# Kernel tuning notes

Measured on AMD Instinct MI355X. Metric: run time of the kernel, lower is better.

The kernel has to match this reference:

```python
import jax, jax.numpy as jnp
import numpy as np

B, S = 32, 10  # hard-coded in original call()/reshape


def setup_inputs() -> dict:
    key = jax.random.key(0)
    k1, k2, k3 = jax.random.split(key, 3)
    D, K = 4096, 8192
    p = jax.random.normal(k1, (B, S, D), dtype=jnp.float32)
    q = jax.random.normal(k2, (B, S, D), dtype=jnp.float32)
    W = jax.random.uniform(k3, (K, D), dtype=jnp.float32)  # 'uniform' initializer
    return {"p": p, "q": q, "W": W}


def reference(p, q, W):
    # Multi-perspective matching: for each perspective k, weight p rows and the
    # last q state by W[k], then cosine distance = -mean(l2norm(a)*l2norm(b)).
    # Vectorized over (batch, perspective, seq) via einsums on W^2 -- never
    # materializes the (B,K,S,D) weighted tensors.
    D = p.shape[-1]
    W2 = W * W                                   # (K, D)
    q_last = q[:, -1, :]                          # (B, D)
    # dot(w*q_last, w*p_s) = sum_d p*q_last*W^2
    dot = jnp.einsum('bsd,kd->bks', p * q_last[:, None, :], W2)   # (B, K, S)
    norm_p = jnp.sqrt(jnp.einsum('bsd,kd->bks', p * p, W2))       # (B, K, S)
    norm_q = jnp.sqrt(jnp.einsum('bd,kd->bk', q_last * q_last, W2))  # (B, K)
    dist = -dot / (norm_p * norm_q[:, :, None] * D)  # -mean of normalized product
    # original concatenates over k then s per batch, then reshapes to (32,10,K)
    return dist.reshape(B, S, -1)
```

## Files before the change

kernel.cpp:

```cpp
#include <hip/hip_runtime.h>
#include <stdint.h>

#define B_ 32
#define S_ 10
#define D_ 4096
#define K_ 8192
#define RPB 21
#define M_REAL (B_ * RPB)

#define BM 128
#define BN 128
#define BK 32
#define M_PAD_MF 768
#define KSPLIT 2
#define KHALF (D_ / KSPLIT)
#define NSTEP (KHALF / BK)

typedef _Float16 f16x8 __attribute__((ext_vector_type(8)));
typedef float f32x4 __attribute__((ext_vector_type(4)));
typedef unsigned short us4 __attribute__((ext_vector_type(4)));

__device__ __forceinline__ void async16(const void* g, void* l) {
  __builtin_amdgcn_global_load_lds(
      (const __attribute__((address_space(1))) unsigned int*)g,
      (__attribute__((address_space(3))) unsigned int*)l, 16, 0, 0);
}

__global__ __launch_bounds__(256)
void build_a_f16(const float* __restrict__ p, const float* __restrict__ q,
                 unsigned short* __restrict__ Af) {
  size_t idx = (size_t)blockIdx.x * 256 + threadIdx.x;
  int d4 = (int)(idx & 1023);
  int m = (int)(idx >> 10);
  float4 v = make_float4(0.f, 0.f, 0.f, 0.f);
  if (m < M_REAL) {
    int b = m / RPB;
    int r = m - b * RPB;
    const float4* q4 = (const float4*)(q + (size_t)(b * S_ + (S_ - 1)) * D_);
    if (r < S_) {
      const float4* p4 = (const float4*)(p + (size_t)(b * S_ + r) * D_);
      float4 pv = p4[d4]; float4 qv = q4[d4];
      v = make_float4(pv.x * qv.x, pv.y * qv.y, pv.z * qv.z, pv.w * qv.w);
    } else if (r < 2 * S_) {
      const float4* p4 = (const float4*)(p + (size_t)(b * S_ + (r - S_)) * D_);
      float4 pv = p4[d4];
      v = make_float4(pv.x * pv.x, pv.y * pv.y, pv.z * pv.z, pv.w * pv.w);
    } else {
      float4 qv = q4[d4];
      v = make_float4(qv.x * qv.x, qv.y * qv.y, qv.z * qv.z, qv.w * qv.w);
    }
  }
  us4 h;
  ((unsigned short*)&h)[0] = (unsigned short)__builtin_bit_cast(unsigned short, (_Float16)v.x);
  ((unsigned short*)&h)[1] = (unsigned short)__builtin_bit_cast(unsigned short, (_Float16)v.y);
  ((unsigned short*)&h)[2] = (unsigned short)__builtin_bit_cast(unsigned short, (_Float16)v.z);
  ((unsigned short*)&h)[3] = (unsigned short)__builtin_bit_cast(unsigned short, (_Float16)v.w);
  ((us4*)Af)[idx] = h;
}

__global__ __launch_bounds__(256, 4)
void gemm_mfma(const unsigned short* __restrict__ Af, const float* __restrict__ W,
               float* __restrict__ G) {
  __shared__ unsigned short lds[24576];
  const int tid = threadIdx.x;
  const int lane = tid & 63;
  const int wid = tid >> 6;
  const int m0 = blockIdx.y * BM;
  const int n0 = blockIdx.x * BN;
  const int ks = blockIdx.z;
  const int d_base = ks * KHALF;

  char* const ldsb = (char*)lds;
  char* const ldsWf = ldsb + 16384;

  const unsigned short* gpA[2];
  uint32_t ldsoffA[2];
#pragma unroll
  for (int half = 0; half < 2; ++half) {
    int row = half * 64 + wid * 16 + (lane >> 2);
    int g = (lane & 3) ^ ((row ^ (row >> 2)) & 3);
    gpA[half] = Af + (size_t)(m0 + row) * D_ + d_base + g * 8;
    ldsoffA[half] = (uint32_t)(half * 4096 + wid * 1024);
  }

  const float* gpW[4];
  uint32_t ldsoffW[4];
#pragma unroll
  for (int e = 0; e < 4; ++e) {
    int row = wid * 32 + e * 8 + (lane >> 3);
    int g = (lane & 7) ^ (row & 7);
    gpW[e] = W + (size_t)(n0 + row) * D_ + d_base + g * 4;
    ldsoffW[e] = (uint32_t)((wid * 4 + e) * 1024);
  }

  f32x4 acc[4][4];
#pragma unroll
  for (int i = 0; i < 4; ++i)
#pragma unroll
    for (int j = 0; j < 4; ++j) acc[i][j] = (f32x4){0.f, 0.f, 0.f, 0.f};

  const int wm = wid >> 1;
  const int wn = wid & 1;
  const int frow = lane & 15;
  const int k16 = lane >> 4;
  int aoff[4];
  int woffL[4], woffH[4];
#pragma unroll
  for (int f = 0; f < 4; ++f) {
    int ra = wm * 64 + f * 16 + frow;
    aoff[f] = ra * 64 + ((k16 ^ ((ra ^ (ra >> 2)) & 3)) * 16);
    int rw = wn * 64 + f * 16 + frow;
    woffL[f] = rw * 128 + (((2 * k16) ^ (rw & 7)) * 16);
    woffH[f] = rw * 128 + (((2 * k16 + 1) ^ (rw & 7)) * 16);
  }

  async16(gpA[0], ldsb + ldsoffA[0]);
  async16(gpA[1], ldsb + ldsoffA[1]);
#pragma unroll
  for (int e = 0; e < 4; ++e) async16(gpW[e], ldsWf + ldsoffW[e]);
  __syncthreads();

  for (int i = 0; i < NSTEP; ++i) {
    const int dn = ((i + 1 < NSTEP) ? (i + 1) : i) * BK;
    const uint32_t nbA = (uint32_t)(((i + 1) & 1) * 8192);
    const uint32_t nbW = (uint32_t)(((i + 1) & 1) * 16384);
    async16(gpA[0] + dn, ldsb + nbA + ldsoffA[0]);
    async16(gpA[1] + dn, ldsb + nbA + ldsoffA[1]);
#pragma unroll
    for (int e = 0; e < 4; ++e)
      async16(gpW[e] + dn, ldsWf + nbW + ldsoffW[e]);

    const uint32_t cbA = (uint32_t)((i & 1) * 8192);
    const uint32_t cbW = (uint32_t)((i & 1) * 16384);
    f16x8 aF[4];
#pragma unroll
    for (int f = 0; f < 4; ++f)
      aF[f] = *(const f16x8*)(ldsb + cbA + aoff[f]);
#pragma unroll
    for (int nf = 0; nf < 4; ++nf) {
      f32x4 lo = *(const f32x4*)(ldsWf + cbW + woffL[nf]);
      f32x4 hi = *(const f32x4*)(ldsWf + cbW + woffH[nf]);
      f16x8 wF;
      wF[0] = (_Float16)(lo[0] * lo[0]); wF[1] = (_Float16)(lo[1] * lo[1]);
      wF[2] = (_Float16)(lo[2] * lo[2]); wF[3] = (_Float16)(lo[3] * lo[3]);
      wF[4] = (_Float16)(hi[0] * hi[0]); wF[5] = (_Float16)(hi[1] * hi[1]);
      wF[6] = (_Float16)(hi[2] * hi[2]); wF[7] = (_Float16)(hi[3] * hi[3]);
#pragma unroll
      for (int mf = 0; mf < 4; ++mf)
        acc[mf][nf] = __builtin_amdgcn_mfma_f32_16x16x32_f16(aF[mf], wF, acc[mf][nf], 0, 0, 0);
    }

    __syncthreads();
  }

  float* Gp = G + (size_t)ks * M_PAD_MF * K_;
  const int crow = m0 + wm * 64;
  const int ccol = n0 + wn * 64;
#pragma unroll
  for (int mf = 0; mf < 4; ++mf)
#pragma unroll
    for (int nf = 0; nf < 4; ++nf)
#pragma unroll
      for (int r = 0; r < 4; ++r) {
        int row = crow + mf * 16 + (lane >> 4) * 4 + r;
        int col = ccol + nf * 16 + (lane & 15);
        Gp[(size_t)row * K_ + col] = acc[mf][nf][r];
      }
}

__global__ __launch_bounds__(256)
void epilogue2(const float* __restrict__ G, float* __restrict__ out) {
  __shared__ float buf[256 * S_];
  const int tid = threadIdx.x;
  const int b = blockIdx.y;
  const int k0 = blockIdx.x * 256;
  const int k = k0 + tid;
  const float* G0 = G + (size_t)b * RPB * K_ + k;
  const float* G1 = G0 + (size_t)M_PAD_MF * K_;
  float nq = sqrtf(G0[20 * K_] + G1[20 * K_]);
#pragma unroll
  for (int s = 0; s < S_; ++s) {
    float dot = G0[s * K_] + G1[s * K_];
    float pp = G0[(S_ + s) * K_] + G1[(S_ + s) * K_];
    buf[tid * S_ + s] = -dot / (sqrtf(pp) * nq * (float)D_);
  }
  __syncthreads();
  float* ob = out + ((size_t)b * K_ + k0) * S_;
  for (int i = tid; i < 256 * S_; i += 256) ob[i] = buf[i];
}

extern "C" void kernel_launch(void* const* d_in, const int* in_sizes, int n_in,
                              void* d_out, int out_size, void* d_ws, size_t ws_size,
                              hipStream_t stream) {
  const float* p = (const float*)d_in[0];
  const float* q = (const float*)d_in[1];
  const float* W = (const float*)d_in[2];
  float* out = (float*)d_out;

  uint8_t* w = (uint8_t*)d_ws;
  unsigned short* Af = (unsigned short*)w;
  float* G = (float*)(w + 6291456);

  build_a_f16<<<(M_PAD_MF * (D_ / 4)) / 256, 256, 0, stream>>>(p, q, Af);
  dim3 ggrid(K_ / BN, M_PAD_MF / BM, KSPLIT);
  gemm_mfma<<<ggrid, 256, 0, stream>>>(Af, W, G);
  epilogue2<<<dim3(K_ / 256, B_), 256, 0, stream>>>(G, out);
}
```

Before: 128.0 us.

## Double GEMM M-tile to 256 with 8 waves and split K four ways

The GEMM block grows to 512 threads covering a 256x128 output tile, so each fp32 W tile is loaded and squared for twice as many A rows. This halves how many times the large W matrix is streamed. The K split goes from two to four to keep the grid at 768 blocks, and the epilogue now sums four partial planes. In exchange, the partial-sum buffer doubles in size, which means more global writes and epilogue reads and a larger workspace requirement. The 512-thread launch bound may also tighten register limits.

```diff
diff --git a/kernel.cpp b/kernel.cpp
--- a/kernel.cpp
+++ b/kernel.cpp
@@ -8,13 +8,13 @@
 #define RPB 21
 #define M_REAL (B_ * RPB)
 
-#define BM 128
+#define BM 256
 #define BN 128
 #define BK 32
 #define M_PAD_MF 768
-#define KSPLIT 2
-#define KHALF (D_ / KSPLIT)
-#define NSTEP (KHALF / BK)
+#define KSPLIT 4
+#define KCHUNK (D_ / KSPLIT)
+#define NSTEP (KCHUNK / BK)
 
 typedef _Float16 f16x8 __attribute__((ext_vector_type(8)));
 typedef float f32x4 __attribute__((ext_vector_type(4)));
@@ -58,39 +58,41 @@
   ((us4*)Af)[idx] = h;
 }
 
-__global__ __launch_bounds__(256, 4)
+__global__ __launch_bounds__(512, 4)
 void gemm_mfma(const unsigned short* __restrict__ Af, const float* __restrict__ W,
                float* __restrict__ G) {
-  __shared__ unsigned short lds[24576];
+  __shared__ unsigned short lds[32768];
   const int tid = threadIdx.x;
   const int lane = tid & 63;
   const int wid = tid >> 6;
   const int m0 = blockIdx.y * BM;
   const int n0 = blockIdx.x * BN;
   const int ks = blockIdx.z;
-  const int d_base = ks * KHALF;
+  const int d_base = ks * KCHUNK;
 
   char* const ldsb = (char*)lds;
-  char* const ldsWf = ldsb + 16384;
+  char* const ldsWf = ldsb + 32768;
 
   const unsigned short* gpA[2];
   uint32_t ldsoffA[2];
 #pragma unroll
-  for (int half = 0; half < 2; ++half) {
-    int row = half * 64 + wid * 16 + (lane >> 2);
-    int g = (lane & 3) ^ ((row ^ (row >> 2)) & 3);
-    gpA[half] = Af + (size_t)(m0 + row) * D_ + d_base + g * 8;
-    ldsoffA[half] = (uint32_t)(half * 4096 + wid * 1024);
-  }
-
-  const float* gpW[4];
-  uint32_t ldsoffW[4];
-#pragma unroll
-  for (int e = 0; e < 4; ++e) {
-    int row = wid * 32 + e * 8 + (lane >> 3);
-    int g = (lane & 7) ^ (row & 7);
+  for (int e = 0; e < 2; ++e) {
+    int c = e * 512 + tid;
+    int row = c >> 2;
+    int g = (tid & 3) ^ ((row ^ (row >> 2)) & 3);
+    gpA[e] = Af + (size_t)(m0 + row) * D_ + d_base + g * 8;
+    ldsoffA[e] = (uint32_t)(e * 8192 + wid * 1024);
+  }
+
+  const float* gpW[2];
+  uint32_t ldsoffW[2];
+#pragma unroll
+  for (int e = 0; e < 2; ++e) {
+    int c = e * 512 + tid;
+    int row = c >> 3;
+    int g = (tid & 7) ^ (row & 7);
     gpW[e] = W + (size_t)(n0 + row) * D_ + d_base + g * 4;
-    ldsoffW[e] = (uint32_t)((wid * 4 + e) * 1024);
+    ldsoffW[e] = (uint32_t)(e * 8192 + wid * 1024);
   }
 
   f32x4 acc[4][4];
@@ -116,30 +118,27 @@
 
   async16(gpA[0], ldsb + ldsoffA[0]);
   async16(gpA[1], ldsb + ldsoffA[1]);
-#pragma unroll
-  for (int e = 0; e < 4; ++e) async16(gpW[e], ldsWf + ldsoffW[e]);
+  async16(gpW[0], ldsWf + ldsoffW[0]);
+  async16(gpW[1], ldsWf + ldsoffW[1]);
   __syncthreads();
 
   for (int i = 0; i < NSTEP; ++i) {
     const int dn = ((i + 1 < NSTEP) ? (i + 1) : i) * BK;
-    const uint32_t nbA = (uint32_t)(((i + 1) & 1) * 8192);
-    const uint32_t nbW = (uint32_t)(((i + 1) & 1) * 16384);
-    async16(gpA[0] + dn, ldsb + nbA + ldsoffA[0]);
-    async16(gpA[1] + dn, ldsb + nbA + ldsoffA[1]);
-#pragma unroll
-    for (int e = 0; e < 4; ++e)
-      async16(gpW[e] + dn, ldsWf + nbW + ldsoffW[e]);
-
-    const uint32_t cbA = (uint32_t)((i & 1) * 8192);
-    const uint32_t cbW = (uint32_t)((i & 1) * 16384);
+    const uint32_t nb = (uint32_t)(((i + 1) & 1) * 16384);
+    async16(gpA[0] + dn, ldsb + nb + ldsoffA[0]);
+    async16(gpA[1] + dn, ldsb + nb + ldsoffA[1]);
+    async16(gpW[0] + dn, ldsWf + nb + ldsoffW[0]);
+    async16(gpW[1] + dn, ldsWf + nb + ldsoffW[1]);
+
+    const uint32_t cb = (uint32_t)((i & 1) * 16384);
     f16x8 aF[4];
 #pragma unroll
     for (int f = 0; f < 4; ++f)
-      aF[f] = *(const f16x8*)(ldsb + cbA + aoff[f]);
+      aF[f] = *(const f16x8*)(ldsb + cb + aoff[f]);
 #pragma unroll
     for (int nf = 0; nf < 4; ++nf) {
-      f32x4 lo = *(const f32x4*)(ldsWf + cbW + woffL[nf]);
-      f32x4 hi = *(const f32x4*)(ldsWf + cbW + woffH[nf]);
+      f32x4 lo = *(const f32x4*)(ldsWf + cb + woffL[nf]);
+      f32x4 hi = *(const f32x4*)(ldsWf + cb + woffH[nf]);
       f16x8 wF;
       wF[0] = (_Float16)(lo[0] * lo[0]); wF[1] = (_Float16)(lo[1] * lo[1]);
       wF[2] = (_Float16)(lo[2] * lo[2]); wF[3] = (_Float16)(lo[3] * lo[3]);
@@ -169,19 +168,21 @@
 }
 
 __global__ __launch_bounds__(256)
-void epilogue2(const float* __restrict__ G, float* __restrict__ out) {
+void epilogue4(const float* __restrict__ G, float* __restrict__ out) {
   __shared__ float buf[256 * S_];
   const int tid = threadIdx.x;
   const int b = blockIdx.y;
   const int k0 = blockIdx.x * 256;
   const int k = k0 + tid;
-  const float* G0 = G + (size_t)b * RPB * K_ + k;
-  const float* G1 = G0 + (size_t)M_PAD_MF * K_;
-  float nq = sqrtf(G0[20 * K_] + G1[20 * K_]);
+  const size_t PL = (size_t)M_PAD_MF * K_;
+  const float* Gb = G + (size_t)b * RPB * K_ + k;
+  float nq = sqrtf(Gb[20 * K_] + Gb[PL + 20 * K_] + Gb[2 * PL + 20 * K_] + Gb[3 * PL + 20 * K_]);
 #pragma unroll
   for (int s = 0; s < S_; ++s) {
-    float dot = G0[s * K_] + G1[s * K_];
-    float pp = G0[(S_ + s) * K_] + G1[(S_ + s) * K_];
+    size_t od = (size_t)s * K_;
+    size_t op = (size_t)(S_ + s) * K_;
+    float dot = Gb[od] + Gb[PL + od] + Gb[2 * PL + od] + Gb[3 * PL + od];
+    float pp  = Gb[op] + Gb[PL + op] + Gb[2 * PL + op] + Gb[3 * PL + op];
     buf[tid * S_ + s] = -dot / (sqrtf(pp) * nq * (float)D_);
   }
   __syncthreads();
@@ -203,6 +204,6 @@
 
   build_a_f16<<<(M_PAD_MF * (D_ / 4)) / 256, 256, 0, stream>>>(p, q, Af);
   dim3 ggrid(K_ / BN, M_PAD_MF / BM, KSPLIT);
-  gemm_mfma<<<ggrid, 256, 0, stream>>>(Af, W, G);
-  epilogue2<<<dim3(K_ / 256, B_), 256, 0, stream>>>(G, out);
-}
+  gemm_mfma<<<ggrid, 512, 0, stream>>>(Af, W, G);
+  epilogue4<<<dim3(K_ / 256, B_), 256, 0, stream>>>(G, out);
+}
```

New measurement: 121.0 us (median of 2 runs). 1.06x faster.

## Triple-buffer GEMM LDS stages with partial vmcnt waits for deeper prefetch

Applied to the files above, without the earlier changes.

Moves the GEMM main loop from double to triple buffering in LDS, issuing loads two steps ahead. Each iteration waits only until the oldest stage has arrived (vmcnt(6)) before the barrier, instead of draining all loads with __syncthreads. This is meant to hide global-load latency behind the MFMA work. In exchange LDS use grows to 72KB and the occupancy hint in launch_bounds is dropped, which may lower the number of resident blocks per CU.

```diff
diff --git a/kernel.cpp b/kernel.cpp
--- a/kernel.cpp
+++ b/kernel.cpp
@@ -58,10 +58,10 @@
   ((us4*)Af)[idx] = h;
 }
 
-__global__ __launch_bounds__(256, 4)
+__global__ __launch_bounds__(256)
 void gemm_mfma(const unsigned short* __restrict__ Af, const float* __restrict__ W,
                float* __restrict__ G) {
-  __shared__ unsigned short lds[24576];
+  __shared__ unsigned short lds[36864];
   const int tid = threadIdx.x;
   const int lane = tid & 63;
   const int wid = tid >> 6;
@@ -71,7 +71,7 @@
   const int d_base = ks * KHALF;
 
   char* const ldsb = (char*)lds;
-  char* const ldsWf = ldsb + 16384;
+  char* const ldsWf = ldsb + 24576;
 
   const unsigned short* gpA[2];
   uint32_t ldsoffA[2];
@@ -114,32 +114,40 @@
     woffH[f] = rw * 128 + (((2 * k16 + 1) ^ (rw & 7)) * 16);
   }
 
-  async16(gpA[0], ldsb + ldsoffA[0]);
-  async16(gpA[1], ldsb + ldsoffA[1]);
-#pragma unroll
-  for (int e = 0; e < 4; ++e) async16(gpW[e], ldsWf + ldsoffW[e]);
-  __syncthreads();
+#define STAGE_STEP(dstep, bslot)                                        \
+  {                                                                     \
+    const int _d = (dstep) * BK;                                        \
+    char* _ab = ldsb + (bslot) * 8192;                                  \
+    char* _wb = ldsWf + (bslot) * 16384;                                \
+    async16(gpA[0] + _d, _ab + ldsoffA[0]);                             \
+    async16(gpA[1] + _d, _ab + ldsoffA[1]);                             \
+    async16(gpW[0] + _d, _wb + ldsoffW[0]);                             \
+    async16(gpW[1] + _d, _wb + ldsoffW[1]);                             \
+    async16(gpW[2] + _d, _wb + ldsoffW[2]);                             \
+    async16(gpW[3] + _d, _wb + ldsoffW[3]);                             \
+  }
+
+  STAGE_STEP(0, 0);
+  STAGE_STEP(1, 1);
+  __builtin_amdgcn_sched_barrier(0);
+  asm volatile("s_waitcnt vmcnt(6)" ::: "memory");
+  __builtin_amdgcn_s_barrier();
+  __builtin_amdgcn_sched_barrier(0);
 
   for (int i = 0; i < NSTEP; ++i) {
-    const int dn = ((i + 1 < NSTEP) ? (i + 1) : i) * BK;
-    const uint32_t nbA = (uint32_t)(((i + 1) & 1) * 8192);
-    const uint32_t nbW = (uint32_t)(((i + 1) & 1) * 16384);
-    async16(gpA[0] + dn, ldsb + nbA + ldsoffA[0]);
-    async16(gpA[1] + dn, ldsb + nbA + ldsoffA[1]);
-#pragma unroll
-    for (int e = 0; e < 4; ++e)
-      async16(gpW[e] + dn, ldsWf + nbW + ldsoffW[e]);
-
-    const uint32_t cbA = (uint32_t)((i & 1) * 8192);
-    const uint32_t cbW = (uint32_t)((i & 1) * 16384);
+    const int ds = (i + 2 < NSTEP) ? (i + 2) : (NSTEP - 1);
+    STAGE_STEP(ds, (i + 2) % 3);
+
+    char* const cbA = ldsb + (i % 3) * 8192;
+    char* const cbW = ldsWf + (i % 3) * 16384;
     f16x8 aF[4];
 #pragma unroll
     for (int f = 0; f < 4; ++f)
-      aF[f] = *(const f16x8*)(ldsb + cbA + aoff[f]);
+      aF[f] = *(const f16x8*)(cbA + aoff[f]);
 #pragma unroll
     for (int nf = 0; nf < 4; ++nf) {
-      f32x4 lo = *(const f32x4*)(ldsWf + cbW + woffL[nf]);
-      f32x4 hi = *(const f32x4*)(ldsWf + cbW + woffH[nf]);
+      f32x4 lo = *(const f32x4*)(cbW + woffL[nf]);
+      f32x4 hi = *(const f32x4*)(cbW + woffH[nf]);
       f16x8 wF;
       wF[0] = (_Float16)(lo[0] * lo[0]); wF[1] = (_Float16)(lo[1] * lo[1]);
       wF[2] = (_Float16)(lo[2] * lo[2]); wF[3] = (_Float16)(lo[3] * lo[3]);
@@ -150,8 +158,12 @@
         acc[mf][nf] = __builtin_amdgcn_mfma_f32_16x16x32_f16(aF[mf], wF, acc[mf][nf], 0, 0, 0);
     }
 
-    __syncthreads();
-  }
+    __builtin_amdgcn_sched_barrier(0);
+    asm volatile("s_waitcnt vmcnt(6)" ::: "memory");
+    __builtin_amdgcn_s_barrier();
+    __builtin_amdgcn_sched_barrier(0);
+  }
+#undef STAGE_STEP
 
   float* Gp = G + (size_t)ks * M_PAD_MF * K_;
   const int crow = m0 + wm * 64;
```

After: 134.9 us. +5.3%, slower.
